# Performance work log

Measured on AMD Instinct MI355X. Metric: run time of the kernel, lower is better.

The kernel has to match this reference:

```python
import jax, jax.numpy as jnp
import numpy as np

TASKS = 32768          # init kwarg `tasks`
N_HEADS = TASKS + 1    # tasks + 1 distilled/shared head
IN_DIM, HID, OUT = 3, 100, 5


def setup_inputs() -> dict:
    key = jax.random.key(0)
    kx, k1, kb1, k2, kb2 = jax.random.split(key, 5)
    # per-task stacked parameters (equivalent to ModuleList of Linears)
    x = jax.random.normal(kx, (N_HEADS, IN_DIM), dtype=jnp.float32)
    # init scale ~ PyTorch default: U(-1/sqrt(fan_in), 1/sqrt(fan_in)); gaussian approx fine
    W1 = jax.random.normal(k1, (N_HEADS, HID, IN_DIM), dtype=jnp.float32) * (1.0 / np.sqrt(IN_DIM))
    b1 = jax.random.normal(kb1, (N_HEADS, HID), dtype=jnp.float32) * (1.0 / np.sqrt(IN_DIM))
    W2 = jax.random.normal(k2, (N_HEADS, OUT, HID), dtype=jnp.float32) * (1.0 / np.sqrt(HID))
    b2 = jax.random.normal(kb2, (N_HEADS, OUT), dtype=jnp.float32) * (1.0 / np.sqrt(HID))
    return {"x": x, "W1": W1, "b1": b1, "W2": W2, "b2": b2}


def reference(x, W1, b1, W2, b2):
    # x: (T+1, 3) -- one state vector per task head (matches x.view(tasks+1, -1))
    T1 = W1.shape[0]
    x = x.reshape(T1, -1)                                   # (T+1, 3)
    h = jax.nn.relu(jnp.einsum('thi,ti->th', W1, x) + b1)   # (T+1, 100)
    logits = jnp.einsum('toh,th->to', W2, h) + b2           # (T+1, 5)
    return jax.nn.softmax(logits, axis=-1)                  # (T+1, 5)
```

## Files before the change

kernel.cpp:

```cpp
#include <hip/hip_runtime.h>
#include <math.h>


#define N_HEADS 32769
#define HID     100
#define OUT     5
#define CHUNKS  25
#define PART    4100
#define BLK_PER_PART 513

__global__ __launch_bounds__(256) void distral_kernel(
    const float* __restrict__ x,
    const float* __restrict__ W1,
    const float* __restrict__ b1,
    const float* __restrict__ W2,
    const float* __restrict__ b2,
    float* __restrict__ out)
{
    const int lane = threadIdx.x & 63;
    const int half = lane >> 5;
    const int ll   = lane & 31;
    const int wv   = threadIdx.x >> 6;

    const int p    = blockIdx.x & 7;
    const int i    = blockIdx.x >> 3;
    const int slot = i * 8 + wv * 2 + half;
    const int hraw = p * PART + slot;
    const bool valid = (slot < PART) && (hraw < N_HEADS);
    const int  head  = valid ? hraw : (N_HEADS - 1);

    const int c = (ll < CHUNKS) ? ll : (CHUNKS - 1);
    const bool active = (ll < CHUNKS);

    const float4* W1q = (const float4*)(W1 + (size_t)head * 300);
    const float4* b1q = (const float4*)(b1 + (size_t)head * 100);
    const float4* W2q = (const float4*)(W2 + (size_t)head * 500);

    const float4 q0 = W1q[3 * c + 0];
    const float4 q1 = W1q[3 * c + 1];
    const float4 q2 = W1q[3 * c + 2];
    const float4 bq = b1q[c];
    float4 w2[OUT];
#pragma unroll
    for (int o = 0; o < OUT; ++o)
        w2[o] = W2q[CHUNKS * o + c];

    const float x0 = x[head * 3 + 0];
    const float x1 = x[head * 3 + 1];
    const float x2 = x[head * 3 + 2];
    float b2v[OUT];
#pragma unroll
    for (int o = 0; o < OUT; ++o) b2v[o] = b2[head * OUT + o];

    const float h0 = fmaxf(fmaf(q0.x, x0, fmaf(q0.y, x1, fmaf(q0.z, x2, bq.x))), 0.f);
    const float h1 = fmaxf(fmaf(q0.w, x0, fmaf(q1.x, x1, fmaf(q1.y, x2, bq.y))), 0.f);
    const float h2 = fmaxf(fmaf(q1.z, x0, fmaf(q1.w, x1, fmaf(q2.x, x2, bq.z))), 0.f);
    const float h3 = fmaxf(fmaf(q2.y, x0, fmaf(q2.z, x1, fmaf(q2.w, x2, bq.w))), 0.f);

    float logit[OUT];
#pragma unroll
    for (int o = 0; o < OUT; ++o) {
        float pt = fmaf(h0, w2[o].x, fmaf(h1, w2[o].y,
                   fmaf(h2, w2[o].z, h3 * w2[o].w)));
        pt = active ? pt : 0.0f;
#pragma unroll
        for (int m = 16; m > 0; m >>= 1)
            pt += __shfl_xor(pt, m, 64);
        logit[o] = pt + b2v[o];
    }

    float mx = -INFINITY;
#pragma unroll
    for (int o = 0; o < OUT; ++o) mx = fmaxf(mx, logit[o]);
    float e[OUT], s = 0.0f;
#pragma unroll
    for (int o = 0; o < OUT; ++o) { e[o] = __expf(logit[o] - mx); s += e[o]; }
    const float inv = 1.0f / s;

    if (valid && ll < OUT) {
        float v = (ll == 0) ? e[0]
                : (ll == 1) ? e[1]
                : (ll == 2) ? e[2]
                : (ll == 3) ? e[3]
                :             e[4];
        out[(size_t)head * OUT + ll] = v * inv;
    }
}

extern "C" void kernel_launch(void* const* d_in, const int* in_sizes, int n_in,
                              void* d_out, int out_size, void* d_ws, size_t ws_size,
                              hipStream_t stream) {
    const float* x  = (const float*)d_in[0];
    const float* W1 = (const float*)d_in[1];
    const float* b1 = (const float*)d_in[2];
    const float* W2 = (const float*)d_in[3];
    const float* b2 = (const float*)d_in[4];
    float* out = (float*)d_out;

    distral_kernel<<<8 * BLK_PER_PART, 256, 0, stream>>>(x, W1, b1, W2, b2, out);
}
```

Measured before the change: 143.4 us.

## Stage per-block head weights into LDS via direct global-to-LDS loads

Each block now cooperatively copies the contiguous W1, b1 and W2 slices for its 8 heads into shared memory using global_load_lds with 16-byte per-lane transfers, then syncs and reads the per-lane float4 operands from LDS. Previously each lane issued strided float4 global loads, with 7 of every 32 lanes idle. The aim is fully coalesced, dense loads that avoid wasted lanes and register staging. In exchange it adds 30 KB of LDS per block, which may limit occupancy, plus a block barrier.

New measurement: 144.7 us. No clear change (+0.9%).

```diff
diff --git a/kernel.cpp b/kernel.cpp
--- a/kernel.cpp
+++ b/kernel.cpp
@@ -5,7 +5,6 @@
 #define N_HEADS 32769
 #define HID     100
 #define OUT     5
-#define CHUNKS  25
 #define PART    4100
 #define BLK_PER_PART 513
 
@@ -17,40 +16,76 @@
     const float* __restrict__ b2,
     float* __restrict__ out)
 {
-    const int lane = threadIdx.x & 63;
+    __shared__ __align__(16) float lds[7680];
+
+    const int tid  = threadIdx.x;
+    const int lane = tid & 63;
+    const int wv   = tid >> 6;
     const int half = lane >> 5;
     const int ll   = lane & 31;
-    const int wv   = threadIdx.x >> 6;
 
-    const int p    = blockIdx.x & 7;
-    const int i    = blockIdx.x >> 3;
-    const int slot = i * 8 + wv * 2 + half;
-    const int hraw = p * PART + slot;
+    const int p  = blockIdx.x & 7;
+    const int i  = blockIdx.x >> 3;
+    const int H0 = p * PART + i * 8;
+
+    const size_t W1len = (size_t)N_HEADS * 300;
+    const size_t b1len = (size_t)N_HEADS * 100;
+    const size_t W2len = (size_t)N_HEADS * 500;
+
+#pragma unroll
+    for (int j = 0; j < 8; ++j) {
+        const int k = j * 4 + wv;
+        if (k < 30) {
+            const float* base;
+            size_t srcf, len;
+            int dst;
+            if (k < 10) {
+                base = W1; srcf = (size_t)H0 * 300 + (size_t)k * 256;
+                dst  = k * 256;              len = W1len;
+            } else if (k < 14) {
+                base = b1; srcf = (size_t)H0 * 100 + (size_t)(k - 10) * 256;
+                dst  = 2560 + (k - 10) * 256; len = b1len;
+            } else {
+                base = W2; srcf = (size_t)H0 * 500 + (size_t)(k - 14) * 256;
+                dst  = 3584 + (k - 14) * 256; len = W2len;
+            }
+            size_t sf = srcf + (size_t)(lane * 4);
+            const size_t lim = len - 4;
+            if (sf > lim) sf = lim;
+            __builtin_amdgcn_global_load_lds(
+                (const __attribute__((address_space(1))) unsigned int*)(base + sf),
+                (__attribute__((address_space(3))) unsigned int*)(&lds[dst]),
+                16, 0, 0);
+        }
+    }
+
+    const int hl   = wv * 2 + half;
+    const int slot = i * 8 + hl;
+    const int hraw = H0 + hl;
     const bool valid = (slot < PART) && (hraw < N_HEADS);
     const int  head  = valid ? hraw : (N_HEADS - 1);
-
-    const int c = (ll < CHUNKS) ? ll : (CHUNKS - 1);
-    const bool active = (ll < CHUNKS);
-
-    const float4* W1q = (const float4*)(W1 + (size_t)head * 300);
-    const float4* b1q = (const float4*)(b1 + (size_t)head * 100);
-    const float4* W2q = (const float4*)(W2 + (size_t)head * 500);
-
-    const float4 q0 = W1q[3 * c + 0];
-    const float4 q1 = W1q[3 * c + 1];
-    const float4 q2 = W1q[3 * c + 2];
-    const float4 bq = b1q[c];
-    float4 w2[OUT];
-#pragma unroll
-    for (int o = 0; o < OUT; ++o)
-        w2[o] = W2q[CHUNKS * o + c];
 
     const float x0 = x[head * 3 + 0];
     const float x1 = x[head * 3 + 1];
     const float x2 = x[head * 3 + 2];
     float b2v[OUT];
 #pragma unroll
-    for (int o = 0; o < OUT; ++o) b2v[o] = b2[head * OUT + o];
+    for (int o = 0; o < OUT; ++o) b2v[o] = b2[(size_t)head * OUT + o];
+
+    __syncthreads();
+
+    const int c = (ll < 25) ? ll : 24;
+    const bool active = (ll < 25);
+
+    const float4* W1v = (const float4*)&lds[hl * 300 + 12 * c];
+    const float4 q0 = W1v[0];
+    const float4 q1 = W1v[1];
+    const float4 q2 = W1v[2];
+    const float4 bq = *(const float4*)&lds[2560 + hl * 100 + 4 * c];
+    float4 w2r[OUT];
+#pragma unroll
+    for (int o = 0; o < OUT; ++o)
+        w2r[o] = *(const float4*)&lds[3584 + hl * 500 + 100 * o + 4 * c];
 
     const float h0 = fmaxf(fmaf(q0.x, x0, fmaf(q0.y, x1, fmaf(q0.z, x2, bq.x))), 0.f);
     const float h1 = fmaxf(fmaf(q0.w, x0, fmaf(q1.x, x1, fmaf(q1.y, x2, bq.y))), 0.f);
@@ -60,8 +95,8 @@
     float logit[OUT];
 #pragma unroll
     for (int o = 0; o < OUT; ++o) {
-        float pt = fmaf(h0, w2[o].x, fmaf(h1, w2[o].y,
-                   fmaf(h2, w2[o].z, h3 * w2[o].w)));
+        float pt = fmaf(h0, w2r[o].x, fmaf(h1, w2r[o].y,
+                   fmaf(h2, w2r[o].z, h3 * w2r[o].w)));
         pt = active ? pt : 0.0f;
 #pragma unroll
         for (int m = 16; m > 0; m >>= 1)
```
